# Optimization experiments

Measured on AMD Instinct MI355X. Metric: run time of the kernel, lower is better.

Reference implementation:

```python
import jax, jax.numpy as jnp
import numpy as np
import math

D_MODEL = 512
N_HEAD = 8
D_FF = 2048
B, S, S_ENC = 2, 2048, 2048
EPS = 1e-5


def _linear_params(key, d_in, d_out):
    kw, kb = jax.random.split(key)
    w = jax.random.normal(kw, (d_in, d_out), dtype=jnp.float32) * 0.02
    b = jax.random.normal(kb, (d_out,), dtype=jnp.float32) * 0.02
    return w, b


def setup_inputs() -> dict:
    key = jax.random.key(0)
    ks = jax.random.split(key, 16)
    dec = jax.random.normal(ks[0], (B, S, D_MODEL), dtype=jnp.float32)
    enc = jax.random.normal(ks[1], (B, S_ENC, D_MODEL), dtype=jnp.float32)
    src_mask = jnp.ones((B, 1, 1, S_ENC), dtype=jnp.int32)  # no padding
    tgt_mask = jnp.tril(jnp.ones((S, S), dtype=jnp.int32))[None, None]  # causal
    inp = {"dec": dec, "enc": enc, "src_mask": src_mask, "tgt_mask": tgt_mask}
    # self-attention projections
    for i, nm in enumerate(["sa_wq", "sa_wk", "sa_wv", "sa_wo"]):
        w, b = _linear_params(ks[2 + i], D_MODEL, D_MODEL)
        inp[nm], inp[nm.replace("w", "b")] = w, b
    # cross-attention projections
    for i, nm in enumerate(["ca_wq", "ca_wk", "ca_wv", "ca_wo"]):
        w, b = _linear_params(ks[6 + i], D_MODEL, D_MODEL)
        inp[nm], inp[nm.replace("w", "b")] = w, b
    # FFN
    inp["ffn_w1"], inp["ffn_b1"] = _linear_params(ks[10], D_MODEL, D_FF)
    inp["ffn_w2"], inp["ffn_b2"] = _linear_params(ks[11], D_FF, D_MODEL)
    # LayerNorms (gamma=1, beta=0 init as in torch)
    for i in (1, 2, 3):
        inp[f"ln{i}_g"] = jnp.ones((D_MODEL,), dtype=jnp.float32)
        inp[f"ln{i}_b"] = jnp.zeros((D_MODEL,), dtype=jnp.float32)
    return inp


def _layer_norm(x, g, b):
    mu = jnp.mean(x, axis=-1, keepdims=True)
    var = jnp.mean(jnp.square(x - mu), axis=-1, keepdims=True)
    return (x - mu) * jax.lax.rsqrt(var + EPS) * g + b


def _mha(xq, xkv, wq, bq, wk, bk, wv, bv, wo, bo, mask):
    Bq, Sq, D = xq.shape
    Sk = xkv.shape[1]
    d_k = D // N_HEAD
    def split(x, s):
        return x.reshape(x.shape[0], s, N_HEAD, d_k).transpose(0, 2, 1, 3)  # [B,H,S,dk]
    q = split(xq @ wq + bq, Sq)
    k = split(xkv @ wk + bk, Sk)
    v = split(xkv @ wv + bv, Sk)
    scores = jnp.einsum("bhqd,bhkd->bhqk", q, k) / math.sqrt(d_k)
    if mask is not None:
        scores = jnp.where(mask == 0, jnp.float32(-1e9), scores)
    attn = jax.nn.softmax(scores, axis=-1)
    out = jnp.einsum("bhqk,bhkd->bhqd", attn, v)
    out = out.transpose(0, 2, 1, 3).reshape(Bq, Sq, D)
    return out @ wo + bo


def reference(dec, enc, src_mask, tgt_mask,
              sa_wq, sa_bq, sa_wk, sa_bk, sa_wv, sa_bv, sa_wo, sa_bo,
              ca_wq, ca_bq, ca_wk, ca_bk, ca_wv, ca_bv, ca_wo, ca_bo,
              ffn_w1, ffn_b1, ffn_w2, ffn_b2,
              ln1_g, ln1_b, ln2_g, ln2_b, ln3_g, ln3_b):
    # dropout is identity in eval mode
    x = _mha(dec, dec, sa_wq, sa_bq, sa_wk, sa_bk, sa_wv, sa_bv, sa_wo, sa_bo, tgt_mask)
    x = _layer_norm(x + dec, ln1_g, ln1_b)
    _x = x
    x = _mha(x, enc, ca_wq, ca_bq, ca_wk, ca_bk, ca_wv, ca_bv, ca_wo, ca_bo, src_mask)
    x = _layer_norm(x + _x, ln2_g, ln2_b)
    _x = x
    x = jax.nn.relu(x @ ffn_w1 + ffn_b1) @ ffn_w2 + ffn_b2
    x = _layer_norm(x + _x, ln3_g, ln3_b)
    return x
```

## Files before the change

kernel.cpp:

```cpp
#include <hip/hip_runtime.h>


#define D_MODEL 512
#define NHEAD 8
#define DK 64
#define SEQ 2048
#define MTOK 4096
#define DFF 2048

typedef __attribute__((ext_vector_type(8))) short bf16x8;
typedef __attribute__((ext_vector_type(4))) float f32x4;

#if __has_builtin(__builtin_amdgcn_exp2f)
#define EXP2(x) __builtin_amdgcn_exp2f(x)
#else
#define EXP2(x) exp2f(x)
#endif

__device__ __forceinline__ unsigned short f2bf(float x) {
  unsigned u = __float_as_uint(x);
  u += 0x7FFF + ((u >> 16) & 1);
  return (unsigned short)(u >> 16);
}
__device__ __forceinline__ unsigned pack2(float a, float b) {
  return (unsigned)f2bf(a) | ((unsigned)f2bf(b) << 16);
}
__device__ __forceinline__ unsigned cvtpk(float lo, float hi) {
  unsigned r;
  asm("v_cvt_pk_bf16_f32 %0, %1, %2" : "=v"(r) : "v"(lo), "v"(hi));
  return r;
}
__device__ __forceinline__ void load_lds16(const unsigned short* g, unsigned short* l) {
  __builtin_amdgcn_global_load_lds(
      (const __attribute__((address_space(1))) void*)g,
      (__attribute__((address_space(3))) void*)l, 16, 0, 0);
}

struct WDesc { const float* src; unsigned short* dst; int K; int N; };
struct WPack { WDesc d[10]; };

__global__ __launch_bounds__(256)
void wprep_kernel(WPack p) {
  const WDesc wd = p.d[blockIdx.y];
  const int ntx = wd.N >> 5;
  const int ntile = (wd.K >> 5) * ntx;
  if ((int)blockIdx.x >= ntile) return;
  const int n0 = (blockIdx.x % ntx) * 32;
  const int k0 = (blockIdx.x / ntx) * 32;
  __shared__ float T[32][33];
  const int tid = threadIdx.x;
  {
    const int r = tid >> 3, c4 = (tid & 7) * 4;
    float4 v = *(const float4*)(wd.src + (long)(k0 + r) * wd.N + n0 + c4);
    T[r][c4] = v.x; T[r][c4 + 1] = v.y; T[r][c4 + 2] = v.z; T[r][c4 + 3] = v.w;
  }
  __syncthreads();
  {
    const int n = tid >> 3, kq = (tid & 7) * 4;
    ushort4 o;
    o.x = f2bf(T[kq + 0][n]); o.y = f2bf(T[kq + 1][n]);
    o.z = f2bf(T[kq + 2][n]); o.w = f2bf(T[kq + 3][n]);
    *(ushort4*)(wd.dst + (long)(n0 + n) * wd.K + k0 + kq) = o;
  }
}

__global__ __launch_bounds__(256)
void cast_kernel(const float* __restrict__ s, unsigned short* __restrict__ d, int n8) {
  const int i = blockIdx.x * 256 + threadIdx.x;
  if (i >= n8) return;
  float4 a = *(const float4*)(s + (long)i * 8);
  float4 b = *(const float4*)(s + (long)i * 8 + 4);
  uint4 o;
  o.x = pack2(a.x, a.y); o.y = pack2(a.z, a.w);
  o.z = pack2(b.x, b.y); o.w = pack2(b.z, b.w);
  *(uint4*)(d + (long)i * 8) = o;
}

template<int MODE, int BM, int BN>
__global__ __launch_bounds__(256)
void gemm_bf16(const unsigned short* __restrict__ A, const unsigned short* __restrict__ Wt,
               const float* __restrict__ b0, const float* __restrict__ b1,
               const float* __restrict__ b2, const float* res,
               const float* __restrict__ lnm, const float* __restrict__ lnr,
               const float* __restrict__ lng, const float* __restrict__ lnbt,
               unsigned short* __restrict__ o0, unsigned short* __restrict__ o1,
               unsigned short* __restrict__ o2, float* of,
               int M, int N, int K, float scale0) {
  constexpr int MF = BM / 32, NF = BN / 32;
  constexpr int AI = BM / 32;
  constexpr int BI = BN / 32;
  __shared__ unsigned short As0[BM * 64];
  __shared__ unsigned short As1[BM * 64];
  __shared__ unsigned short Bs0[BN * 64];
  __shared__ unsigned short Bs1[BN * 64];
  const int tid = threadIdx.x;
  const int w = tid >> 6, lane = tid & 63, g = lane >> 4, li = lane & 15;
  const int m0 = blockIdx.x * BM, n0 = blockIdx.y * BN;
  const int wm = w >> 1, wn = w & 1;

  f32x4 acc[MF][NF] = {};
  const unsigned short* Ap[AI];
  const unsigned short* Bp[BI];
#pragma unroll
  for (int i = 0; i < AI; i++) {
    const int idx = i * 256 + tid;
    Ap[i] = A + (long)(m0 + (idx % BM)) * K + (idx / BM) * 8;
  }
#pragma unroll
  for (int i = 0; i < BI; i++) {
    const int idx = i * 256 + tid;
    Bp[i] = Wt + (long)(n0 + (idx % BN)) * K + (idx / BN) * 8;
  }
  const int nt = K >> 6;

#define G_STAGE(t, Ad, Bd)                                               \
  {                                                                      \
    _Pragma("unroll") for (int i = 0; i < AI; i++)                       \
        load_lds16(Ap[i] + (t) * 64, &Ad[(i * 256 + w * 64) * 8]);       \
    _Pragma("unroll") for (int i = 0; i < BI; i++)                       \
        load_lds16(Bp[i] + (t) * 64, &Bd[(i * 256 + w * 64) * 8]);       \
  }

#define G_COMP(Ad, Bd)                                                            \
  {                                                                               \
    _Pragma("unroll") for (int s = 0; s < 2; s++) {                               \
      bf16x8 af[MF], bfr[NF];                                                     \
      _Pragma("unroll") for (int mf = 0; mf < MF; mf++)                           \
          af[mf] = *(const bf16x8*)&Ad[((s * 4 + g) * BM + wm * (BM / 2) + mf * 16 + li) * 8]; \
      _Pragma("unroll") for (int nf = 0; nf < NF; nf++)                           \
          bfr[nf] = *(const bf16x8*)&Bd[((s * 4 + g) * BN + wn * (BN / 2) + nf * 16 + li) * 8]; \
      _Pragma("unroll") for (int mf = 0; mf < MF; mf++)                           \
          _Pragma("unroll") for (int nf = 0; nf < NF; nf++)                       \
              acc[mf][nf] = __builtin_amdgcn_mfma_f32_16x16x32_bf16(af[mf], bfr[nf], acc[mf][nf], 0, 0, 0); \
    }                                                                             \
  }

  G_STAGE(0, As0, Bs0);
  __syncthreads();
  for (int t = 0; t < nt; t += 2) {
    if (t + 1 < nt) G_STAGE(t + 1, As1, Bs1);
    G_COMP(As0, Bs0);
    __syncthreads();
    if (t + 1 < nt) {
      if (t + 2 < nt) G_STAGE(t + 2, As0, Bs0);
      G_COMP(As1, Bs1);
      __syncthreads();
    }
  }
#undef G_STAGE
#undef G_COMP

#pragma unroll
  for (int nf = 0; nf < NF; nf++) {
    const int c = n0 + wn * (BN / 2) + nf * 16 + li;
    float bias, scl = 1.f;
    unsigned short* hdst = nullptr;
    float lngv = 0.f, lnbv = 0.f;
    if constexpr (MODE == 0) {
      const int which = c >> 9;
      bias = (which == 0 ? b0 : (which == 1 ? b1 : b2))[c & 511];
      if (which == 0) scl = scale0;
      hdst = which == 0 ? o0 : (which == 1 ? o1 : o2);
    } else {
      bias = b0[c];
      if constexpr (MODE == 3) { lngv = lng[c]; lnbv = lnbt[c]; }
    }
#pragma unroll
    for (int mf = 0; mf < MF; mf++) {
#pragma unroll
      for (int j = 0; j < 4; j++) {
        const int r = m0 + wm * (BM / 2) + mf * 16 + g * 4 + j;
        float v = acc[mf][nf][j] + bias;
        if constexpr (MODE == 0) {
          v *= scl;
          const int b = r >> 11, s = r & (SEQ - 1), h = (c >> 6) & 7, d = c & 63;
          hdst[(((long)(b * NHEAD + h)) * SEQ + s) * DK + d] = f2bf(v);
        } else if constexpr (MODE == 1) {
          v += res[(long)r * N + c];
          of[(long)r * N + c] = v;
        } else if constexpr (MODE == 2) {
          o0[(long)r * N + c] = f2bf(fmaxf(v, 0.f));
        } else {
          const float xr = res[(long)r * N + c];
          v += (xr - lnm[r]) * lnr[r] * lngv + lnbv;
          of[(long)r * N + c] = v;
        }
      }
    }
  }
}

template<bool CAUSAL>
__global__ __launch_bounds__(256)
void attn_bf16(const unsigned short* __restrict__ Qg, const unsigned short* __restrict__ Kg,
               const unsigned short* __restrict__ Vg, float* __restrict__ Opart,
               float* __restrict__ Mst, float* __restrict__ Lst) {
  __shared__ unsigned short SM[16384];
  unsigned short* const Qp = SM;
  unsigned short* const Kp = SM + 8192;
  unsigned short* const Vt = SM + 12288;
  const int tid = threadIdx.x;
  const int w = tid >> 6, lane = tid & 63, g = lane >> 4, li = lane & 15;
  const int qb = blockIdx.x, bh = blockIdx.y, ck = blockIdx.z;
  const int q0 = qb * 128;
  const long base = (long)bh * SEQ * DK;
  unsigned short* const Pl = SM + w * 2048;

#pragma unroll
  for (int i = 0; i < 4; i++) {
    const int idx = i * 256 + tid;
    const int dg = idx >> 7, q = idx & 127;
    load_lds16(Qg + base + (long)(q0 + q) * DK + dg * 8, &Qp[(i * 256 + w * 64) * 8]);
  }
  __syncthreads();
  bf16x8 bq[2][2];
#pragma unroll
  for (int qf = 0; qf < 2; qf++)
#pragma unroll
    for (int ks = 0; ks < 2; ks++)
      bq[qf][ks] = *(const bf16x8*)&Qp[((ks * 4 + g) * 128 + w * 32 + qf * 16 + li) * 8];

  f32x4 oacc[2][4] = {};
  float mrun[2] = {-1e30f, -1e30f};
  float denom[2] = {0.f, 0.f};

  const int vdg = tid >> 5;
  const int vs0 = (tid & 31) * 2;
  const int vsg = vs0 >> 3, vso = vs0 & 7;

  const int tbeg = CAUSAL ? ck : ck * 8;
  const int tend = CAUSAL ? (2 * qb + 2) : (ck * 8 + 8);
  const int tstep = CAUSAL ? 4 : 1;
  for (int t = tbeg; t < tend; t += tstep) {
    const int k0 = t * 64;
    __syncthreads();
#pragma unroll
    for (int i = 0; i < 2; i++) {
      const int idx = i * 256 + tid;
      const int dg = idx >> 6, kk = idx & 63;
      load_lds16(Kg + base + (long)(k0 + kk) * DK + dg * 8, &Kp[(i * 256 + w * 64) * 8]);
    }
    {
      const unsigned short* vsrc = Vg + base + (long)(k0 + vs0) * DK + vdg * 8;
      uint4 r0 = *(const uint4*)vsrc;
      uint4 r1 = *(const uint4*)(vsrc + DK);
      unsigned short u0[8], u1[8];
      *(uint4*)u0 = r0; *(uint4*)u1 = r1;
#pragma unroll
      for (int e = 0; e < 8; e++) {
        const int d = vdg * 8 + e;
        const int dsw = d ^ (vsg & 7);
        *(unsigned*)&Vt[(vsg * 64 + dsw) * 8 + vso] =
            (unsigned)u0[e] | ((unsigned)u1[e] << 16);
      }
    }
    __syncthreads();

    f32x4 sacc[4][2] = {};
#pragma unroll
    for (int ks = 0; ks < 2; ks++) {
#pragma unroll
      for (int kf = 0; kf < 4; kf++) {
        bf16x8 ka = *(const bf16x8*)&Kp[((ks * 4 + g) * 64 + kf * 16 + li) * 8];
#pragma unroll
        for (int qf = 0; qf < 2; qf++)
          sacc[kf][qf] = __builtin_amdgcn_mfma_f32_16x16x32_bf16(ka, bq[qf][ks], sacc[kf][qf], 0, 0, 0);
      }
    }
    if (CAUSAL && t >= 2 * qb) {
#pragma unroll
      for (int kf = 0; kf < 4; kf++)
#pragma unroll
        for (int qf = 0; qf < 2; qf++)
#pragma unroll
          for (int j = 0; j < 4; j++) {
            const int kg_ = k0 + kf * 16 + g * 4 + j;
            const int qg_ = q0 + w * 32 + qf * 16 + li;
            if (kg_ > qg_) sacc[kf][qf][j] = -1e30f;
          }
    }
    float mx[2];
#pragma unroll
    for (int qf = 0; qf < 2; qf++) {
      float a = fmaxf(fmaxf(sacc[0][qf][0], sacc[0][qf][1]), fmaxf(sacc[0][qf][2], sacc[0][qf][3]));
      float b = fmaxf(fmaxf(sacc[1][qf][0], sacc[1][qf][1]), fmaxf(sacc[1][qf][2], sacc[1][qf][3]));
      float c = fmaxf(fmaxf(sacc[2][qf][0], sacc[2][qf][1]), fmaxf(sacc[2][qf][2], sacc[2][qf][3]));
      float d = fmaxf(fmaxf(sacc[3][qf][0], sacc[3][qf][1]), fmaxf(sacc[3][qf][2], sacc[3][qf][3]));
      float m_ = fmaxf(fmaxf(a, b), fmaxf(c, d));
      m_ = fmaxf(m_, __shfl_xor(m_, 16, 64));
      m_ = fmaxf(m_, __shfl_xor(m_, 32, 64));
      mx[qf] = m_;
    }
    const int full = !__all((mx[0] - mrun[0] <= 8.f) && (mx[1] - mrun[1] <= 8.f));
    float corrv[2] = {1.f, 1.f};
    if (full) {
#pragma unroll
      for (int qf = 0; qf < 2; qf++) {
        const float mn = fmaxf(mrun[qf], mx[qf]);
        corrv[qf] = EXP2(mrun[qf] - mn);
        mrun[qf] = mn;
      }
    }
#pragma unroll
    for (int qf = 0; qf < 2; qf++) {
      float ps = 0.f;
#pragma unroll
      for (int kf = 0; kf < 4; kf++)
#pragma unroll
        for (int j = 0; j < 4; j++) {
          const float p = EXP2(sacc[kf][qf][j] - mrun[qf]);
          sacc[kf][qf][j] = p;
          ps += p;
        }
      ps += __shfl_xor(ps, 16, 64);
      ps += __shfl_xor(ps, 32, 64);
      denom[qf] = denom[qf] * corrv[qf] + ps;
    }
    if (full) {
#pragma unroll
      for (int mf = 0; mf < 2; mf++)
#pragma unroll
        for (int j = 0; j < 4; j++) {
          const float cf = __shfl(corrv[mf], g * 4 + j, 64);
#pragma unroll
          for (int df = 0; df < 4; df++) oacc[mf][df][j] *= cf;
        }
    }
#pragma unroll
    for (int kf = 0; kf < 4; kf++)
#pragma unroll
      for (int qf = 0; qf < 2; qf++) {
        uint2 pv;
        pv.x = cvtpk(sacc[kf][qf][0], sacc[kf][qf][1]);
        pv.y = cvtpk(sacc[kf][qf][2], sacc[kf][qf][3]);
        *(uint2*)&Pl[((kf * 2 + (g >> 1)) * 32 + qf * 16 + li) * 8 + (g & 1) * 4] = pv;
      }
#pragma unroll
    for (int ks2 = 0; ks2 < 2; ks2++) {
      const int sg = ks2 * 4 + g;
#pragma unroll
      for (int mf = 0; mf < 2; mf++) {
        bf16x8 pa = *(const bf16x8*)&Pl[(sg * 32 + mf * 16 + li) * 8];
#pragma unroll
        for (int df = 0; df < 4; df++) {
          bf16x8 vb = *(const bf16x8*)&Vt[(sg * 64 + ((df * 16 + li) ^ (sg & 7))) * 8];
          oacc[mf][df] = __builtin_amdgcn_mfma_f32_16x16x32_bf16(pa, vb, oacc[mf][df], 0, 0, 0);
        }
      }
    }
  }

  const long pbase = (long)(ck * 16 + bh) * SEQ;
  if (g == 0) {
#pragma unroll
    for (int qf = 0; qf < 2; qf++) {
      const int q = q0 + w * 32 + qf * 16 + li;
      Mst[pbase + q] = mrun[qf];
      Lst[pbase + q] = denom[qf];
    }
  }
#pragma unroll
  for (int mf = 0; mf < 2; mf++)
#pragma unroll
    for (int j = 0; j < 4; j++) {
      const int q = q0 + w * 32 + mf * 16 + g * 4 + j;
      float* op = Opart + (pbase + q) * 64;
#pragma unroll
      for (int df = 0; df < 4; df++) op[df * 16 + li] = oacc[mf][df][j];
    }
}

__global__ __launch_bounds__(256)
void combine_kernel(const float* __restrict__ Opart, const float* __restrict__ Mst,
                    const float* __restrict__ Lst, unsigned short* __restrict__ AOb) {
  const int row = blockIdx.x * 4 + (threadIdx.x >> 6);
  const int lane = threadIdx.x & 63;
  const int bh = row >> 11, q = row & (SEQ - 1);
  float m[4], l[4], mstar = -1e30f;
#pragma unroll
  for (int c = 0; c < 4; c++) {
    m[c] = Mst[((long)c * 16 + bh) * SEQ + q];
    l[c] = Lst[((long)c * 16 + bh) * SEQ + q];
    mstar = fmaxf(mstar, m[c]);
  }
  float den = 0.f, o = 0.f;
#pragma unroll
  for (int c = 0; c < 4; c++) {
    const float wgt = EXP2(m[c] - mstar);
    den += wgt * l[c];
    o += wgt * Opart[(((long)c * 16 + bh) * SEQ + q) * 64 + lane];
  }
  const int b = bh >> 3, h = bh & 7;
  AOb[((long)(b * SEQ + q)) * D_MODEL + h * DK + lane] = f2bf(o / den);
}

template<int V>
__global__ __launch_bounds__(256)
void ln_kernel(const float* __restrict__ x, const float* __restrict__ gam,
               const float* __restrict__ bet, float* __restrict__ outf,
               unsigned short* __restrict__ outb, float* __restrict__ mu_s,
               float* __restrict__ rs_s) {
  const int row = blockIdx.x * 4 + (threadIdx.x >> 6);
  const int lane = threadIdx.x & 63;
  const float* xr = x + (long)row * D_MODEL;
  float4 v0 = *(const float4*)&xr[lane * 8];
  float4 v1 = *(const float4*)&xr[lane * 8 + 4];
  float xv[8] = {v0.x, v0.y, v0.z, v0.w, v1.x, v1.y, v1.z, v1.w};
  float s = 0.f, s2 = 0.f;
#pragma unroll
  for (int i = 0; i < 8; i++) { s += xv[i]; s2 = fmaf(xv[i], xv[i], s2); }
#pragma unroll
  for (int off = 32; off > 0; off >>= 1) {
    s += __shfl_xor(s, off, 64);
    s2 += __shfl_xor(s2, off, 64);
  }
  const float mu = s * (1.f / D_MODEL);
  const float var = fmaxf(s2 * (1.f / D_MODEL) - mu * mu, 0.f);
  const float rstd = rsqrtf(var + 1e-5f);
  float y[8];
#pragma unroll
  for (int i = 0; i < 8; i++) {
    const int c = lane * 8 + i;
    y[i] = (xv[i] - mu) * rstd * gam[c] + bet[c];
  }
  if constexpr (V == 0) {
    uint4 o;
    o.x = pack2(y[0], y[1]); o.y = pack2(y[2], y[3]);
    o.z = pack2(y[4], y[5]); o.w = pack2(y[6], y[7]);
    *(uint4*)(outb + (long)row * D_MODEL + lane * 8) = o;
    if (lane == 0) { mu_s[row] = mu; rs_s[row] = rstd; }
  } else {
    float* orow = outf + (long)row * D_MODEL + lane * 8;
    *(float4*)orow = make_float4(y[0], y[1], y[2], y[3]);
    *(float4*)(orow + 4) = make_float4(y[4], y[5], y[6], y[7]);
  }
}

extern "C" void kernel_launch(void* const* d_in, const int* in_sizes, int n_in,
                              void* d_out, int out_size, void* d_ws, size_t ws_size,
                              hipStream_t stream) {
  const float* dec = (const float*)d_in[0];
  const float* enc = (const float*)d_in[1];
  const float* sa_wq = (const float*)d_in[4];
  const float* sa_bq = (const float*)d_in[5];
  const float* sa_wk = (const float*)d_in[6];
  const float* sa_bk = (const float*)d_in[7];
  const float* sa_wv = (const float*)d_in[8];
  const float* sa_bv = (const float*)d_in[9];
  const float* sa_wo = (const float*)d_in[10];
  const float* sa_bo = (const float*)d_in[11];
  const float* ca_wq = (const float*)d_in[12];
  const float* ca_bq = (const float*)d_in[13];
  const float* ca_wk = (const float*)d_in[14];
  const float* ca_bk = (const float*)d_in[15];
  const float* ca_wv = (const float*)d_in[16];
  const float* ca_bv = (const float*)d_in[17];
  const float* ca_wo = (const float*)d_in[18];
  const float* ca_bo = (const float*)d_in[19];
  const float* ffn_w1 = (const float*)d_in[20];
  const float* ffn_b1 = (const float*)d_in[21];
  const float* ffn_w2 = (const float*)d_in[22];
  const float* ffn_b2 = (const float*)d_in[23];
  const float* ln1_g = (const float*)d_in[24];
  const float* ln1_b = (const float*)d_in[25];
  const float* ln2_g = (const float*)d_in[26];
  const float* ln2_b = (const float*)d_in[27];
  const float* ln3_g = (const float*)d_in[28];
  const float* ln3_b = (const float*)d_in[29];

  char* wsb = (char*)d_ws;
  unsigned short* dec_bf = (unsigned short*)wsb;
  float* Opart = (float*)wsb;
  float* Mst = (float*)(wsb + 33554432);
  float* Lst = (float*)(wsb + 34078720);
  unsigned short* MIDb = (unsigned short*)wsb;
  size_t off = 34603008;
  unsigned short* qkv_t = (unsigned short*)(wsb + off); off += 1572864;
  unsigned short* wo_t  = (unsigned short*)(wsb + off); off += 524288;
  unsigned short* cq_t  = (unsigned short*)(wsb + off); off += 524288;
  unsigned short* ckv_t = (unsigned short*)(wsb + off); off += 1048576;
  unsigned short* co_t  = (unsigned short*)(wsb + off); off += 524288;
  unsigned short* f1_t  = (unsigned short*)(wsb + off); off += 2097152;
  unsigned short* f2_t  = (unsigned short*)(wsb + off); off += 2097152;
  unsigned short* enc_bf = (unsigned short*)(wsb + off); off += 4194304;
  unsigned short* Qb  = (unsigned short*)(wsb + off); off += 4194304;
  unsigned short* Kb  = (unsigned short*)(wsb + off); off += 4194304;
  unsigned short* Vb  = (unsigned short*)(wsb + off); off += 4194304;
  unsigned short* AOb = (unsigned short*)(wsb + off); off += 4194304;
  unsigned short* X1b = (unsigned short*)(wsb + off); off += 4194304;
  unsigned short* X2b = (unsigned short*)(wsb + off); off += 4194304;
  float* R   = (float*)(wsb + off); off += 8388608;
  float* mu1 = (float*)(wsb + off); off += 16384;
  float* rs1 = (float*)(wsb + off); off += 16384;
  float* mu2 = (float*)(wsb + off); off += 16384;
  float* rs2 = (float*)(wsb + off); off += 16384;

  dim3 blk(256);
  const float QS = 0.125f * 1.44269504f;

  WPack wp;
  wp.d[0] = {sa_wq, qkv_t, 512, 512};
  wp.d[1] = {sa_wk, qkv_t + 262144, 512, 512};
  wp.d[2] = {sa_wv, qkv_t + 524288, 512, 512};
  wp.d[3] = {sa_wo, wo_t, 512, 512};
  wp.d[4] = {ca_wq, cq_t, 512, 512};
  wp.d[5] = {ca_wk, ckv_t, 512, 512};
  wp.d[6] = {ca_wv, ckv_t + 262144, 512, 512};
  wp.d[7] = {ca_wo, co_t, 512, 512};
  wp.d[8] = {ffn_w1, f1_t, 512, 2048};
  wp.d[9] = {ffn_w2, f2_t, 2048, 512};
  wprep_kernel<<<dim3(1024, 10), blk, 0, stream>>>(wp);
  cast_kernel<<<1024, blk, 0, stream>>>(dec, dec_bf, 262144);
  cast_kernel<<<1024, blk, 0, stream>>>(enc, enc_bf, 262144);

  gemm_bf16<0, 128, 128><<<dim3(32, 12), blk, 0, stream>>>(dec_bf, qkv_t, sa_bq, sa_bk, sa_bv,
      nullptr, nullptr, nullptr, nullptr, nullptr, Qb, Kb, Vb, nullptr, MTOK, 1536, 512, QS);
  attn_bf16<true><<<dim3(16, 16, 4), blk, 0, stream>>>(Qb, Kb, Vb, Opart, Mst, Lst);
  combine_kernel<<<8192, blk, 0, stream>>>(Opart, Mst, Lst, AOb);
  gemm_bf16<1, 128, 64><<<dim3(32, 8), blk, 0, stream>>>(AOb, wo_t, sa_bo, nullptr, nullptr,
      dec, nullptr, nullptr, nullptr, nullptr, nullptr, nullptr, nullptr, R, MTOK, 512, 512, 1.f);
  ln_kernel<0><<<1024, blk, 0, stream>>>(R, ln1_g, ln1_b, nullptr, X1b, mu1, rs1);

  gemm_bf16<0, 128, 64><<<dim3(32, 8), blk, 0, stream>>>(X1b, cq_t, ca_bq, nullptr, nullptr,
      nullptr, nullptr, nullptr, nullptr, nullptr, Qb, nullptr, nullptr, nullptr, MTOK, 512, 512, QS);
  gemm_bf16<0, 128, 128><<<dim3(32, 8), blk, 0, stream>>>(enc_bf, ckv_t, ca_bk, ca_bv, nullptr,
      nullptr, nullptr, nullptr, nullptr, nullptr, Kb, Vb, nullptr, nullptr, MTOK, 1024, 512, 1.f);
  attn_bf16<false><<<dim3(16, 16, 4), blk, 0, stream>>>(Qb, Kb, Vb, Opart, Mst, Lst);
  combine_kernel<<<8192, blk, 0, stream>>>(Opart, Mst, Lst, AOb);
  gemm_bf16<3, 128, 64><<<dim3(32, 8), blk, 0, stream>>>(AOb, co_t, ca_bo, nullptr, nullptr,
      R, mu1, rs1, ln1_g, ln1_b, nullptr, nullptr, nullptr, R, MTOK, 512, 512, 1.f);
  ln_kernel<0><<<1024, blk, 0, stream>>>(R, ln2_g, ln2_b, nullptr, X2b, mu2, rs2);

  gemm_bf16<2, 128, 128><<<dim3(32, 16), blk, 0, stream>>>(X2b, f1_t, ffn_b1, nullptr, nullptr,
      nullptr, nullptr, nullptr, nullptr, nullptr, MIDb, nullptr, nullptr, nullptr, MTOK, 2048, 512, 1.f);
  gemm_bf16<3, 128, 64><<<dim3(32, 8), blk, 0, stream>>>(MIDb, f2_t, ffn_b2, nullptr, nullptr,
      R, mu2, rs2, ln2_g, ln2_b, nullptr, nullptr, nullptr, R, MTOK, 512, 2048, 1.f);
  ln_kernel<1><<<1024, blk, 0, stream>>>(R, ln3_g, ln3_b, (float*)d_out, nullptr, nullptr, nullptr);
}
```

Measured before the change: 409.2 us.

## Double-buffer K tiles and prefetch V into registers in attention loop

The attention kernel now issues the async LDS load of the next K tile into a second buffer and loads the next V tile into registers before computing the current tile. The V transpose write to LDS is deferred to the end of the iteration, between two barriers. This is meant to hide global memory latency behind the QK and PV MFMA work. In exchange it uses more LDS and more registers (the extra K buffer and the V registers), and keeps two barriers per iteration.

Result: no change. 412.7 us (+0.8%).

```diff
diff --git a/kernel.cpp b/kernel.cpp
--- a/kernel.cpp
+++ b/kernel.cpp
@@ -195,16 +195,51 @@
 void attn_bf16(const unsigned short* __restrict__ Qg, const unsigned short* __restrict__ Kg,
                const unsigned short* __restrict__ Vg, float* __restrict__ Opart,
                float* __restrict__ Mst, float* __restrict__ Lst) {
-  __shared__ unsigned short SM[16384];
-  unsigned short* const Qp = SM;
-  unsigned short* const Kp = SM + 8192;
-  unsigned short* const Vt = SM + 12288;
+  __shared__ unsigned short Qp[8192];
+  __shared__ unsigned short Kp0[4096];
+  __shared__ unsigned short Kp1[4096];
+  __shared__ unsigned short Vt[4096];
   const int tid = threadIdx.x;
   const int w = tid >> 6, lane = tid & 63, g = lane >> 4, li = lane & 15;
   const int qb = blockIdx.x, bh = blockIdx.y, ck = blockIdx.z;
   const int q0 = qb * 128;
   const long base = (long)bh * SEQ * DK;
-  unsigned short* const Pl = SM + w * 2048;
+  unsigned short* const Pl = Qp + w * 2048;
+
+  const int vdg = tid >> 5;
+  const int vs0 = (tid & 31) * 2;
+  const int vsg = vs0 >> 3, vso = vs0 & 7;
+
+  uint4 vr0, vr1;
+  auto kstage = [&](int t, unsigned short* Kd) {
+#pragma unroll
+    for (int i = 0; i < 2; i++) {
+      const int idx = i * 256 + tid;
+      load_lds16(Kg + base + (long)(t * 64 + (idx & 63)) * DK + (idx >> 6) * 8,
+                 &Kd[(i * 256 + w * 64) * 8]);
+    }
+  };
+  auto vload = [&](int t) {
+    const unsigned short* vsrc = Vg + base + (long)(t * 64 + vs0) * DK + vdg * 8;
+    vr0 = *(const uint4*)vsrc;
+    vr1 = *(const uint4*)(vsrc + DK);
+  };
+  auto vwrite = [&]() {
+    unsigned short u0[8], u1[8];
+    *(uint4*)u0 = vr0; *(uint4*)u1 = vr1;
+#pragma unroll
+    for (int e = 0; e < 8; e++) {
+      const int d = vdg * 8 + e;
+      const int dsw = d ^ (vsg & 7);
+      *(unsigned*)&Vt[(vsg * 64 + dsw) * 8 + vso] =
+          (unsigned)u0[e] | ((unsigned)u1[e] << 16);
+    }
+  };
+
+  const int tbeg = CAUSAL ? ck : ck * 8;
+  const int tend = CAUSAL ? (2 * qb + 2) : (ck * 8 + 8);
+  const int tstep = CAUSAL ? 4 : 1;
+  const bool any = tbeg < tend;
 
 #pragma unroll
   for (int i = 0; i < 4; i++) {
@@ -212,6 +247,7 @@
     const int dg = idx >> 7, q = idx & 127;
     load_lds16(Qg + base + (long)(q0 + q) * DK + dg * 8, &Qp[(i * 256 + w * 64) * 8]);
   }
+  if (any) { kstage(tbeg, Kp0); vload(tbeg); }
   __syncthreads();
   bf16x8 bq[2][2];
 #pragma unroll
@@ -219,55 +255,32 @@
 #pragma unroll
     for (int ks = 0; ks < 2; ks++)
       bq[qf][ks] = *(const bf16x8*)&Qp[((ks * 4 + g) * 128 + w * 32 + qf * 16 + li) * 8];
+  if (any) vwrite();
+  __syncthreads();
 
   f32x4 oacc[2][4] = {};
   float mrun[2] = {-1e30f, -1e30f};
   float denom[2] = {0.f, 0.f};
-
-  const int vdg = tid >> 5;
-  const int vs0 = (tid & 31) * 2;
-  const int vsg = vs0 >> 3, vso = vs0 & 7;
-
-  const int tbeg = CAUSAL ? ck : ck * 8;
-  const int tend = CAUSAL ? (2 * qb + 2) : (ck * 8 + 8);
-  const int tstep = CAUSAL ? 4 : 1;
+  unsigned short* Kcur = Kp0;
+  unsigned short* Knxt = Kp1;
+
   for (int t = tbeg; t < tend; t += tstep) {
-    const int k0 = t * 64;
-    __syncthreads();
-#pragma unroll
-    for (int i = 0; i < 2; i++) {
-      const int idx = i * 256 + tid;
-      const int dg = idx >> 6, kk = idx & 63;
-      load_lds16(Kg + base + (long)(k0 + kk) * DK + dg * 8, &Kp[(i * 256 + w * 64) * 8]);
-    }
-    {
-      const unsigned short* vsrc = Vg + base + (long)(k0 + vs0) * DK + vdg * 8;
-      uint4 r0 = *(const uint4*)vsrc;
-      uint4 r1 = *(const uint4*)(vsrc + DK);
-      unsigned short u0[8], u1[8];
-      *(uint4*)u0 = r0; *(uint4*)u1 = r1;
-#pragma unroll
-      for (int e = 0; e < 8; e++) {
-        const int d = vdg * 8 + e;
-        const int dsw = d ^ (vsg & 7);
-        *(unsigned*)&Vt[(vsg * 64 + dsw) * 8 + vso] =
-            (unsigned)u0[e] | ((unsigned)u1[e] << 16);
-      }
-    }
-    __syncthreads();
+    const bool hasnext = (t + tstep) < tend;
+    if (hasnext) { kstage(t + tstep, Knxt); vload(t + tstep); }
 
     f32x4 sacc[4][2] = {};
 #pragma unroll
     for (int ks = 0; ks < 2; ks++) {
 #pragma unroll
       for (int kf = 0; kf < 4; kf++) {
-        bf16x8 ka = *(const bf16x8*)&Kp[((ks * 4 + g) * 64 + kf * 16 + li) * 8];
+        bf16x8 ka = *(const bf16x8*)&Kcur[((ks * 4 + g) * 64 + kf * 16 + li) * 8];
 #pragma unroll
         for (int qf = 0; qf < 2; qf++)
           sacc[kf][qf] = __builtin_amdgcn_mfma_f32_16x16x32_bf16(ka, bq[qf][ks], sacc[kf][qf], 0, 0, 0);
       }
     }
     if (CAUSAL && t >= 2 * qb) {
+      const int k0 = t * 64;
 #pragma unroll
       for (int kf = 0; kf < 4; kf++)
 #pragma unroll
@@ -348,6 +361,11 @@
         }
       }
     }
+
+    __syncthreads();
+    if (hasnext) vwrite();
+    __syncthreads();
+    unsigned short* tmp = Kcur; Kcur = Knxt; Knxt = tmp;
   }
 
   const long pbase = (long)(ck * 16 + bh) * SEQ;
```
